# Performance work log

Measured on AMD Instinct MI355X. Metric: run time of the kernel, lower is better.

Reference implementation:

```python
import jax, jax.numpy as jnp
import numpy as np
from jax import lax

IMSIZE = 64
A_SIZE = 8
C_SIZE = 10
P_SIZE = 100
VI_K = 30
GAMMA = 0.99


def setup_inputs() -> dict:
    key = jax.random.key(0)
    ks = jax.random.split(key, 8)
    B, SB = 32, 128
    S = IMSIZE * IMSIZE
    x = jax.random.normal(ks[0], (B, 2, IMSIZE, IMSIZE), jnp.float32)
    s1 = jax.random.randint(ks[1], (B, SB), 0, IMSIZE)
    s2 = jax.random.randint(ks[2], (B, SB), 0, IMSIZE)
    ds_state = jax.random.randint(ks[3], (S, A_SIZE, C_SIZE), 0, S)
    ds_prob = jax.random.randint(ks[4], (S, A_SIZE, C_SIZE), 0, P_SIZE)
    conv_w = jax.random.normal(ks[5], (1, 2, 3, 3), jnp.float32) * 0.1
    conv_b = jnp.zeros((1,), jnp.float32)
    # original init: arange(P)/max -> values in [0,1]
    pv = jnp.arange(P_SIZE, dtype=jnp.float32) / (P_SIZE - 1)
    lin_w = jax.random.normal(ks[6], (A_SIZE, A_SIZE), jnp.float32) * 0.1
    lin_b = jnp.zeros((A_SIZE,), jnp.float32)
    return dict(x=x, s1=s1, s2=s2, ds_state=ds_state, ds_prob=ds_prob,
                conv_w=conv_w, conv_b=conv_b, pv=pv, lin_w=lin_w, lin_b=lin_b)


def reference(x, s1, s2, ds_state, ds_prob, conv_w, conv_b, pv, lin_w, lin_b):
    B = x.shape[0]
    S = IMSIZE * IMSIZE
    # fr: 3x3 conv, 2->1 channels, SAME padding  -> sar [B, S, 1]
    sar = lax.conv_general_dilated(
        x, conv_w, window_strides=(1, 1), padding='SAME',
        dimension_numbers=('NCHW', 'OIHW', 'NCHW')) + conv_b[None, :, None, None]
    sar = sar.reshape(B, S, 1)
    # sad: done channel / 10 -> [B, S, 1, 1]
    sad = x[:, 1].reshape(B, S, 1, 1) / 10.0
    p = jnp.clip(pv, 0.0, 1.0)
    cf = ds_state.reshape(-1)                                # [S*A*C] successor state ids
    cp = p[ds_prob.reshape(-1)].reshape(1, S, A_SIZE, C_SIZE)  # gathered transition probs
    # torch.max over size-1 dim == squeeze
    v0 = sar[:, :, 0]                                        # [B, S]
    # hoist the per-iteration-constant weight: cp * gamma * (1 - sad)
    w = cp * GAMMA * (1.0 - sad)                             # [B, S, A, C]

    def step(carry, _):
        v, _q = carry
        vc = v[:, cf].reshape(B, S, A_SIZE, C_SIZE)          # gather successor values
        q = sar + jnp.sum(w * vc, axis=3)                    # [B, S, A]
        return (jnp.max(q, axis=2), q), None

    q_init = jnp.zeros((B, S, A_SIZE), x.dtype)
    (v, q), _ = lax.scan(step, (v0, q_init), None, length=VI_K)
    # final residual linear layer over the action dim
    qf = q.reshape(-1, A_SIZE)
    qf = qf @ lin_w.T + lin_b + qf
    q = qf.reshape(B, S, A_SIZE)
    # Q[i, j] = q[i, s1[i,j]*imsize + s2[i,j], :]  (vectorized gather)
    flat = s1 * IMSIZE + s2                                  # [B, state_bs]
    idx = jnp.broadcast_to(flat[:, :, None], flat.shape + (A_SIZE,))
    Q = jnp.take_along_axis(q, idx, axis=1)                  # [B, state_bs, A]
    return Q
```

## Files before the change

kernel.cpp:

```cpp
#include <hip/hip_runtime.h>
#include <math.h>

#define IMSIZE 64
#define S_SIZE 4096
#define A_SZ 8
#define C_SZ 10
#define B_SIZE 32
#define SB 128
#define VI_K 30
#define GAMMA 0.99f


__global__ void init_kernel(const float* __restrict__ x,
                            const float* __restrict__ conv_w,
                            const float* __restrict__ conv_b,
                            float* __restrict__ sar_ws,
                            float* __restrict__ coef_ws,
                            float* __restrict__ v0) {
    int t = blockIdx.x * blockDim.x + threadIdx.x;
    int b = t >> 12;
    int s = t & (S_SIZE - 1);
    int y = s >> 6, xx = s & 63;

    float acc = conv_b[0];
#pragma unroll
    for (int ic = 0; ic < 2; ++ic) {
        const float* xp = x + ((b * 2 + ic) << 12);
#pragma unroll
        for (int ky = 0; ky < 3; ++ky) {
            int yy = y + ky - 1;
            if (yy < 0 || yy >= IMSIZE) continue;
#pragma unroll
            for (int kx = 0; kx < 3; ++kx) {
                int xc = xx + kx - 1;
                if (xc < 0 || xc >= IMSIZE) continue;
                acc += xp[(yy << 6) + xc] * conv_w[(ic * 3 + ky) * 3 + kx];
            }
        }
    }
    float x1 = x[((b * 2 + 1) << 12) + s];
    float coef = GAMMA * (1.0f - x1 * 0.1f);

    int g = b >> 3, b8 = b & 7;
    int o = (((g << 12) + s) << 3) + b8;
    sar_ws[o]  = acc;
    coef_ws[o] = coef;
    v0[o]      = acc;
}

__global__ void pack_kernel(const int* __restrict__ ds_state,
                            const int* __restrict__ ds_prob,
                            const float* __restrict__ pv,
                            int2* __restrict__ pk) {
    int i = blockIdx.x * blockDim.x + threadIdx.x;
    if (i >= S_SIZE * A_SZ * C_SZ) return;
    int idx = ds_state[i];
    float p = pv[ds_prob[i]];
    p = fminf(fmaxf(p, 0.0f), 1.0f);
    int2 e;
    e.x = idx << 3;
    e.y = __float_as_int(p);
    pk[i] = e;
}

__global__ __launch_bounds__(512) void vi_kernel(const float* __restrict__ vin,
                                                 float* __restrict__ vout,
                                                 const float* __restrict__ sar_ws,
                                                 const float* __restrict__ coef_ws,
                                                 const int2* __restrict__ pk) {
    __shared__ float vld[S_SIZE * 8];
    int g = blockIdx.x & 3;
    int slice = blockIdx.x >> 2;
    int tid = threadIdx.x;

    const float4* src = (const float4*)(vin + (g << 15));
    float4* dst = (float4*)vld;
#pragma unroll
    for (int k = 0; k < 16; ++k)
        dst[tid + (k << 9)] = src[tid + (k << 9)];
    __syncthreads();

    int b8 = tid & 7;
    int w = tid >> 3;
    int s = (slice << 6) + w;
    int o = (((g << 12) + s) << 3) + b8;
    float sar = sar_ws[o];
    float coef = coef_ws[o];
    const int2* __restrict__ row = pk + s * (A_SZ * C_SZ);

    float vmax = -INFINITY;
#pragma unroll
    for (int a = 0; a < A_SZ; ++a) {
        float acc = 0.0f;
#pragma unroll
        for (int c = 0; c < C_SZ; ++c) {
            int2 e = row[a * C_SZ + c];
            acc += __int_as_float(e.y) * vld[e.x + b8];
        }
        vmax = fmaxf(vmax, fmaf(coef, acc, sar));
    }
    vout[o] = vmax;
}

__global__ void out_kernel(const float* __restrict__ v29,
                           const float* __restrict__ sar_ws,
                           const float* __restrict__ coef_ws,
                           const int2* __restrict__ pk,
                           const int* __restrict__ s1,
                           const int* __restrict__ s2,
                           const float* __restrict__ lin_w,
                           const float* __restrict__ lin_b,
                           float* __restrict__ out) {
    int t = blockIdx.x * blockDim.x + threadIdx.x;
    if (t >= B_SIZE * SB) return;
    int b = t >> 7;
    int s = s1[t] * IMSIZE + s2[t];
    int g = b >> 3, b8 = b & 7;
    int o = (((g << 12) + s) << 3) + b8;
    float sar = sar_ws[o];
    float coef = coef_ws[o];
    const float* vbase = v29 + (g << 15) + b8;
    const int2* __restrict__ row = pk + s * (A_SZ * C_SZ);

    float q[A_SZ];
#pragma unroll
    for (int a = 0; a < A_SZ; ++a) {
        float acc = 0.0f;
#pragma unroll
        for (int c = 0; c < C_SZ; ++c) {
            int2 e = row[a * C_SZ + c];
            acc += __int_as_float(e.y) * vbase[e.x];
        }
        q[a] = fmaf(coef, acc, sar);
    }
#pragma unroll
    for (int i = 0; i < A_SZ; ++i) {
        float accl = lin_b[i] + q[i];
#pragma unroll
        for (int a = 0; a < A_SZ; ++a)
            accl += q[a] * lin_w[i * 8 + a];
        out[t * 8 + i] = accl;
    }
}

extern "C" void kernel_launch(void* const* d_in, const int* in_sizes, int n_in,
                              void* d_out, int out_size, void* d_ws, size_t ws_size,
                              hipStream_t stream) {
    const float* x       = (const float*)d_in[0];
    const int*   s1      = (const int*)d_in[1];
    const int*   s2      = (const int*)d_in[2];
    const int*   ds_state= (const int*)d_in[3];
    const int*   ds_prob = (const int*)d_in[4];
    const float* conv_w  = (const float*)d_in[5];
    const float* conv_b  = (const float*)d_in[6];
    const float* pv      = (const float*)d_in[7];
    const float* lin_w   = (const float*)d_in[8];
    const float* lin_b   = (const float*)d_in[9];
    float* out = (float*)d_out;

    const size_t VSZ = (size_t)B_SIZE * S_SIZE * 4;
    char* ws = (char*)d_ws;
    float* vA      = (float*)(ws);
    float* vB      = (float*)(ws + VSZ);
    float* sar_ws  = (float*)(ws + 2 * VSZ);
    float* coef_ws = (float*)(ws + 3 * VSZ);
    int2*  pk      = (int2*) (ws + 4 * VSZ);

    init_kernel<<<(B_SIZE * S_SIZE) / 256, 256, 0, stream>>>(
        x, conv_w, conv_b, sar_ws, coef_ws, vA);
    pack_kernel<<<(S_SIZE * A_SZ * C_SZ + 255) / 256, 256, 0, stream>>>(
        ds_state, ds_prob, pv, pk);

    float* vin = vA;
    float* vout = vB;
    for (int i = 0; i < VI_K - 1; ++i) {
        vi_kernel<<<256, 512, 0, stream>>>(vin, vout, sar_ws, coef_ws, pk);
        float* tmp = vin; vin = vout; vout = tmp;
    }

    out_kernel<<<(B_SIZE * SB + 255) / 256, 256, 0, stream>>>(
        vin, sar_ws, coef_ws, pk, s1, s2, lin_w, lin_b, out);
}
```

Baseline: 263.8 us.

## Remap VI threads to state-action pairs with vectorized batch LDS reads

The value-iteration kernel now gives each thread one (state, action) pair and covers all 8 batch lanes at once. It reads successor values as two float4 loads from LDS, using byte offsets prepacked as idx<<5, instead of one scalar load per batch per successor. The max over actions is done with an xor-shuffle reduction inside groups of 8 lanes. The global-to-LDS copy of the value table uses the global_load_lds builtin when available, and the per-thread transition rows, sar and coef are loaded as vectors before the barrier. Because the packed offset encoding changed, out_kernel now reads ds_state, ds_prob and pv directly. The gain comes from far fewer LDS and global load instructions; the cost is extra shuffles and a dependence on the async LDS load being finished at the barrier.

```diff
diff --git a/kernel.cpp b/kernel.cpp
--- a/kernel.cpp
+++ b/kernel.cpp
@@ -34,12 +34,12 @@
             for (int kx = 0; kx < 3; ++kx) {
                 int xc = xx + kx - 1;
                 if (xc < 0 || xc >= IMSIZE) continue;
-                acc += xp[(yy << 6) + xc] * conv_w[(ic * 3 + ky) * 3 + kx];
+                acc = fmaf(xp[(yy << 6) + xc], conv_w[(ic * 3 + ky) * 3 + kx], acc);
             }
         }
     }
     float x1 = x[((b * 2 + 1) << 12) + s];
-    float coef = GAMMA * (1.0f - x1 * 0.1f);
+    float coef = GAMMA * (1.0f - 0.1f * x1);
 
     int g = b >> 3, b8 = b & 7;
     int o = (((g << 12) + s) << 3) + b8;
@@ -58,7 +58,7 @@
     float p = pv[ds_prob[i]];
     p = fminf(fmaxf(p, 0.0f), 1.0f);
     int2 e;
-    e.x = idx << 3;
+    e.x = idx << 5;
     e.y = __float_as_int(p);
     pk[i] = e;
 }
@@ -68,44 +68,103 @@
                                                  const float* __restrict__ sar_ws,
                                                  const float* __restrict__ coef_ws,
                                                  const int2* __restrict__ pk) {
-    __shared__ float vld[S_SIZE * 8];
-    int g = blockIdx.x & 3;
-    int slice = blockIdx.x >> 2;
-    int tid = threadIdx.x;
-
-    const float4* src = (const float4*)(vin + (g << 15));
-    float4* dst = (float4*)vld;
-#pragma unroll
-    for (int k = 0; k < 16; ++k)
-        dst[tid + (k << 9)] = src[tid + (k << 9)];
+    __shared__ float vld[8 * S_SIZE];
+    const int g = blockIdx.x & 3;
+    const int slice = blockIdx.x >> 2;
+    const int tid = threadIdx.x;
+
+    const float4* src4 = (const float4*)(vin + (g << 15));
+    float4* dst4 = (float4*)vld;
+#if __has_builtin(__builtin_amdgcn_global_load_lds)
+#pragma unroll
+    for (int r = 0; r < 16; ++r) {
+        int i = tid + (r << 9);
+        __builtin_amdgcn_global_load_lds(
+            (const __attribute__((address_space(1))) void*)(src4 + i),
+            (__attribute__((address_space(3))) void*)(dst4 + i), 16, 0, 0);
+    }
+#else
+#pragma unroll
+    for (int r = 0; r < 16; ++r) {
+        int i = tid + (r << 9);
+        dst4[i] = src4[i];
+    }
+#endif
+
+    const int w = tid >> 3, a = tid & 7;
+    const int s = (slice << 6) + w;
+
+    int4 er[5];
+    {
+        const int4* rp = (const int4*)(pk + ((s << 3) + a) * C_SZ);
+#pragma unroll
+        for (int i = 0; i < 5; ++i) er[i] = rp[i];
+    }
+    float4 sar_lo, sar_hi, coef_lo, coef_hi;
+    {
+        const float4* sp = (const float4*)(sar_ws + (((g << 12) + s) << 3));
+        const float4* cp = (const float4*)(coef_ws + (((g << 12) + s) << 3));
+        sar_lo = sp[0]; sar_hi = sp[1];
+        coef_lo = cp[0]; coef_hi = cp[1];
+    }
     __syncthreads();
 
-    int b8 = tid & 7;
-    int w = tid >> 3;
-    int s = (slice << 6) + w;
-    int o = (((g << 12) + s) << 3) + b8;
-    float sar = sar_ws[o];
-    float coef = coef_ws[o];
-    const int2* __restrict__ row = pk + s * (A_SZ * C_SZ);
-
-    float vmax = -INFINITY;
-#pragma unroll
-    for (int a = 0; a < A_SZ; ++a) {
-        float acc = 0.0f;
-#pragma unroll
-        for (int c = 0; c < C_SZ; ++c) {
-            int2 e = row[a * C_SZ + c];
-            acc += __int_as_float(e.y) * vld[e.x + b8];
-        }
-        vmax = fmaxf(vmax, fmaf(coef, acc, sar));
-    }
-    vout[o] = vmax;
+    float4 acc_lo = {0.f, 0.f, 0.f, 0.f};
+    float4 acc_hi = {0.f, 0.f, 0.f, 0.f};
+    const char* vbase = (const char*)vld;
+#pragma unroll
+    for (int i = 0; i < 5; ++i) {
+        {
+            int off = er[i].x;
+            float p = __int_as_float(er[i].y);
+            float4 lo = *(const float4*)(vbase + off);
+            float4 hi = *(const float4*)(vbase + off + 16);
+            acc_lo.x = fmaf(p, lo.x, acc_lo.x); acc_lo.y = fmaf(p, lo.y, acc_lo.y);
+            acc_lo.z = fmaf(p, lo.z, acc_lo.z); acc_lo.w = fmaf(p, lo.w, acc_lo.w);
+            acc_hi.x = fmaf(p, hi.x, acc_hi.x); acc_hi.y = fmaf(p, hi.y, acc_hi.y);
+            acc_hi.z = fmaf(p, hi.z, acc_hi.z); acc_hi.w = fmaf(p, hi.w, acc_hi.w);
+        }
+        {
+            int off = er[i].z;
+            float p = __int_as_float(er[i].w);
+            float4 lo = *(const float4*)(vbase + off);
+            float4 hi = *(const float4*)(vbase + off + 16);
+            acc_lo.x = fmaf(p, lo.x, acc_lo.x); acc_lo.y = fmaf(p, lo.y, acc_lo.y);
+            acc_lo.z = fmaf(p, lo.z, acc_lo.z); acc_lo.w = fmaf(p, lo.w, acc_lo.w);
+            acc_hi.x = fmaf(p, hi.x, acc_hi.x); acc_hi.y = fmaf(p, hi.y, acc_hi.y);
+            acc_hi.z = fmaf(p, hi.z, acc_hi.z); acc_hi.w = fmaf(p, hi.w, acc_hi.w);
+        }
+    }
+
+    float q[8];
+    q[0] = fmaf(coef_lo.x, acc_lo.x, sar_lo.x);
+    q[1] = fmaf(coef_lo.y, acc_lo.y, sar_lo.y);
+    q[2] = fmaf(coef_lo.z, acc_lo.z, sar_lo.z);
+    q[3] = fmaf(coef_lo.w, acc_lo.w, sar_lo.w);
+    q[4] = fmaf(coef_hi.x, acc_hi.x, sar_hi.x);
+    q[5] = fmaf(coef_hi.y, acc_hi.y, sar_hi.y);
+    q[6] = fmaf(coef_hi.z, acc_hi.z, sar_hi.z);
+    q[7] = fmaf(coef_hi.w, acc_hi.w, sar_hi.w);
+
+#pragma unroll
+    for (int off = 1; off < 8; off <<= 1) {
+#pragma unroll
+        for (int b = 0; b < 8; ++b)
+            q[b] = fmaxf(q[b], __shfl_xor(q[b], off, 8));
+    }
+    float myv = q[0];
+#pragma unroll
+    for (int b = 1; b < 8; ++b)
+        if (a == b) myv = q[b];
+    vout[(g << 15) + (s << 3) + a] = myv;
 }
 
 __global__ void out_kernel(const float* __restrict__ v29,
+                           const int* __restrict__ ds_state,
+                           const int* __restrict__ ds_prob,
+                           const float* __restrict__ pv,
                            const float* __restrict__ sar_ws,
                            const float* __restrict__ coef_ws,
-                           const int2* __restrict__ pk,
                            const int* __restrict__ s1,
                            const int* __restrict__ s2,
                            const float* __restrict__ lin_w,
@@ -120,42 +179,43 @@
     float sar = sar_ws[o];
     float coef = coef_ws[o];
     const float* vbase = v29 + (g << 15) + b8;
-    const int2* __restrict__ row = pk + s * (A_SZ * C_SZ);
 
     float q[A_SZ];
 #pragma unroll
     for (int a = 0; a < A_SZ; ++a) {
-        float acc = 0.0f;
+        float accq = 0.0f;
+        int bb = (s * A_SZ + a) * C_SZ;
 #pragma unroll
         for (int c = 0; c < C_SZ; ++c) {
-            int2 e = row[a * C_SZ + c];
-            acc += __int_as_float(e.y) * vbase[e.x];
-        }
-        q[a] = fmaf(coef, acc, sar);
+            float p = pv[ds_prob[bb + c]];
+            p = fminf(fmaxf(p, 0.0f), 1.0f);
+            accq = fmaf(p, vbase[ds_state[bb + c] << 3], accq);
+        }
+        q[a] = fmaf(coef, accq, sar);
     }
 #pragma unroll
     for (int i = 0; i < A_SZ; ++i) {
-        float accl = lin_b[i] + q[i];
+        float o2 = lin_b[i] + q[i];
 #pragma unroll
         for (int a = 0; a < A_SZ; ++a)
-            accl += q[a] * lin_w[i * 8 + a];
-        out[t * 8 + i] = accl;
+            o2 = fmaf(q[a], lin_w[i * 8 + a], o2);
+        out[t * 8 + i] = o2;
     }
 }
 
 extern "C" void kernel_launch(void* const* d_in, const int* in_sizes, int n_in,
                               void* d_out, int out_size, void* d_ws, size_t ws_size,
                               hipStream_t stream) {
-    const float* x       = (const float*)d_in[0];
-    const int*   s1      = (const int*)d_in[1];
-    const int*   s2      = (const int*)d_in[2];
-    const int*   ds_state= (const int*)d_in[3];
-    const int*   ds_prob = (const int*)d_in[4];
-    const float* conv_w  = (const float*)d_in[5];
-    const float* conv_b  = (const float*)d_in[6];
-    const float* pv      = (const float*)d_in[7];
-    const float* lin_w   = (const float*)d_in[8];
-    const float* lin_b   = (const float*)d_in[9];
+    const float* x        = (const float*)d_in[0];
+    const int*   s1       = (const int*)d_in[1];
+    const int*   s2       = (const int*)d_in[2];
+    const int*   ds_state = (const int*)d_in[3];
+    const int*   ds_prob  = (const int*)d_in[4];
+    const float* conv_w   = (const float*)d_in[5];
+    const float* conv_b   = (const float*)d_in[6];
+    const float* pv       = (const float*)d_in[7];
+    const float* lin_w    = (const float*)d_in[8];
+    const float* lin_b    = (const float*)d_in[9];
     float* out = (float*)d_out;
 
     const size_t VSZ = (size_t)B_SIZE * S_SIZE * 4;
@@ -179,5 +239,5 @@
     }
 
     out_kernel<<<(B_SIZE * SB + 255) / 256, 256, 0, stream>>>(
-        vin, sar_ws, coef_ws, pk, s1, s2, lin_w, lin_b, out);
-}
+        vin, ds_state, ds_prob, pv, sar_ws, coef_ws, s1, s2, lin_w, lin_b, out);
+}
```

Measured after the change: 271.8 us. 1.03x slower.
